# Optimization experiments

Hardware: AMD Instinct MI355X
Metric: run time of the kernel (lower is better)

Reference implementation:

```python
import jax, jax.numpy as jnp
import numpy as np

S_REF = 2        # number of reference images
C = 1024         # DINOv3 ViT-L channel dim
H = W = 64       # 1024 / patch16 feature resolution
SVD = 500        # positional subspace rank


def _l2norm(x, axis):
    return x / jnp.clip(jnp.linalg.norm(x, axis=axis, keepdims=True), 1e-12)


def setup_inputs() -> dict:
    key = jax.random.key(0)
    k1, k2, k3 = jax.random.split(key, 3)
    fmaps = jax.random.normal(k1, (1, S_REF + 1, C, H, W), jnp.float32)
    ref_masks = jax.random.randint(k2, (S_REF, H, W), 0, 2) > 0  # bool masks at feature res
    basis_raw = jax.random.normal(k3, (C, SVD), jnp.float32)
    basis, _ = jnp.linalg.qr(basis_raw)  # orthonormal positional basis, as SVD U would be
    return {"fmaps": fmaps, "ref_masks": ref_masks, "basis": basis}


def reference(fmaps, ref_masks, basis):
    S = ref_masks.shape[0]
    B, T, Cc, h, w = fmaps.shape

    # F.normalize(fmaps, p=2, dim=2)
    fn = _l2norm(fmaps, 2)
    feat_tgt = fn[0, S]  # (C,h,w) raw-normalized target feats

    # _debias_features: project onto orthogonal complement of positional subspace.
    # (I - U U^T) X computed as X - U (U^T X) to avoid a CxC matrix.
    X = fn.reshape(B * T, Cc, h * w)
    coef = jnp.einsum('ck,bcn->bkn', basis, X)          # (BT, SVD, hw)
    Xd = X - jnp.einsum('ck,bkn->bcn', basis, coef)     # (BT, C, hw)
    fd = _l2norm(Xd.reshape(B, T, Cc, h, w), 2)
    feat_refs_deb = fd[0, :S]   # (S,C,h,w)
    feat_tgt_deb = fd[0, S]     # (C,h,w)

    # Masked feature pooling -> per-reference prototype, then averaged + renormalized
    maskf = ref_masks.astype(fn.dtype)                                  # (S,h,w)
    counts = jnp.clip(maskf.sum(axis=(1, 2)), 1.0)                      # guard empty mask
    protos = jnp.einsum('schw,shw->sc', feat_refs_deb, maskf) / counts[:, None]
    ref_prototype = _l2norm(protos.mean(axis=0), 0)                     # (C,)

    # Dense ref->target cosine-similarity maps: einsum 'bchw,bcxy->bhwxy'
    sim = jnp.einsum('schw,cxy->shwxy', feat_refs_deb, feat_tgt_deb)    # (S,h,w,h,w)

    # Forward matching: target-vs-prototype similarity
    sim_fwd = jnp.einsum('cxy,c->xy', feat_tgt_deb, ref_prototype)      # (h,w)

    # Backward matching votes: for each target patch, argmax over ref patches,
    # vote if the best ref patch lies inside the reference mask.
    sim_t2r = sim.transpose(0, 3, 4, 1, 2).reshape(S, h * w, h * w)     # (S, tgt, ref)
    best_idx = jnp.argmax(sim_t2r, axis=2)                              # (S, hw)
    mask_flat = ref_masks.reshape(S, h * w)
    votes = jnp.take_along_axis(mask_flat, best_idx, axis=1).astype(jnp.int32)
    votes = votes.sum(axis=0).reshape(h, w)                             # (h,w) int32

    return sim, sim_fwd, votes
```

## Files before the change

### kernel.cpp

```cpp
#include <hip/hip_runtime.h>
#include <hip/hip_bf16.h>
#include <cfloat>

#define CH   1024
#define HW   4096
#define NSVD 500
#define TFR  3
#define SREF 2

typedef __attribute__((ext_vector_type(4))) float f32x4;
typedef __attribute__((ext_vector_type(4))) unsigned int u32x4;
typedef __attribute__((ext_vector_type(8))) short short8;


__device__ inline unsigned bfr(float x) {
  unsigned u = __float_as_uint(x);
  return (u + 0x7fffu + ((u >> 16) & 1u)) >> 16;
}
__device__ inline float lores(float x, unsigned h) {
  return x - __uint_as_float(h << 16);
}
__device__ inline float vlo(unsigned ph, unsigned pl) {
  return __uint_as_float(ph << 16) + __uint_as_float(pl << 16);
}
__device__ inline float vhi(unsigned ph, unsigned pl) {
  return __uint_as_float(ph & 0xFFFF0000u) + __uint_as_float(pl & 0xFFFF0000u);
}

__global__ __launch_bounds__(256) void normpack_k(const float* __restrict__ src,
                                                  unsigned* __restrict__ Gh,
                                                  unsigned* __restrict__ Gl,
                                                  int fbase) {
  int t = blockIdx.x >> 6;
  int n0 = (blockIdx.x & 63) * 64;
  int tid = threadIdx.x, nl = tid & 63, r = tid >> 6;
  const float* base = src + (size_t)t * CH * HW + n0 + nl;
  float s = 0.f;
  for (int c = r; c < CH; c += 4) {
    float v = base[(size_t)c * HW];
    s += v * v;
  }
  __shared__ float red[256];
  __shared__ float inv[64];
  red[tid] = s;
  __syncthreads();
  if (r == 0)
    inv[nl] = 1.0f / fmaxf(sqrtf(red[nl] + red[nl + 64] + red[nl + 128] + red[nl + 192]), 1e-12f);
  __syncthreads();

  int cg = (tid & 15) * 4;
  int n4 = n0 + cg;
  float4 w4;
  w4.x = inv[cg]; w4.y = inv[cg + 1]; w4.z = inv[cg + 2]; w4.w = inv[cg + 3];
  int gt = fbase + t;
  for (int kg = tid >> 4; kg < 128; kg += 16) {
    const float* s0 = src + ((size_t)t * CH + kg * 8) * HW + n4;
    unsigned oh[4][4], ol[4][4];
#pragma unroll
    for (int j = 0; j < 4; j++) {
      float4 va = *reinterpret_cast<const float4*>(s0 + (size_t)(2 * j) * HW);
      float4 vb = *reinterpret_cast<const float4*>(s0 + (size_t)(2 * j + 1) * HW);
      float a[4] = {va.x * w4.x, va.y * w4.y, va.z * w4.z, va.w * w4.w};
      float b[4] = {vb.x * w4.x, vb.y * w4.y, vb.z * w4.z, vb.w * w4.w};
#pragma unroll
      for (int cc = 0; cc < 4; cc++) {
        unsigned ha = bfr(a[cc]), hb = bfr(b[cc]);
        oh[cc][j] = ha | (hb << 16);
        ol[cc][j] = bfr(lores(a[cc], ha)) | (bfr(lores(b[cc], hb)) << 16);
      }
    }
    size_t vib = (((size_t)gt * 16 + (n4 >> 8)) * 128 + kg) * 256 + (n4 & 255);
#pragma unroll
    for (int cc = 0; cc < 4; cc++) {
      *reinterpret_cast<u32x4*>(Gh + (vib + cc) * 4) = *reinterpret_cast<u32x4*>(oh[cc]);
      *reinterpret_cast<u32x4*>(Gl + (vib + cc) * 4) = *reinterpret_cast<u32x4*>(ol[cc]);
    }
  }
}

__global__ __launch_bounds__(256) void scale_pack_k(const float* __restrict__ src,
                                                    const float* __restrict__ inv,
                                                    unsigned* __restrict__ Gh,
                                                    unsigned* __restrict__ Gl) {
  int gid = blockIdx.x * 256 + threadIdx.x;
  int kg = gid >> 12;
  int n = gid & 4095;
  const float* s0 = src + (size_t)(kg * 8) * HW + n;
  float w = inv[n];
  unsigned oh[4], ol[4];
#pragma unroll
  for (int j = 0; j < 4; j++) {
    float a = s0[(size_t)(2 * j) * HW] * w;
    float b = s0[(size_t)(2 * j + 1) * HW] * w;
    unsigned ha = bfr(a), hb = bfr(b);
    oh[j] = ha | (hb << 16);
    ol[j] = bfr(lores(a, ha)) | (bfr(lores(b, hb)) << 16);
  }
  size_t vi = (((size_t)(n >> 8)) * 128 + kg) * 256 + (n & 255);
  *reinterpret_cast<u32x4*>(Gh + vi * 4) = *reinterpret_cast<u32x4*>(oh);
  *reinterpret_cast<u32x4*>(Gl + vi * 4) = *reinterpret_cast<u32x4*>(ol);
}

__global__ __launch_bounds__(256) void bt_k(const float* __restrict__ bas,
                                            float* __restrict__ bt) {
  int c0 = blockIdx.x * 64;
  __shared__ float tile[64][129];
  int tid = threadIdx.x;
  for (int kc = 0; kc < 512; kc += 128) {
    for (int cr = tid >> 7; cr < 64; cr += 2) {
      int k = kc + (tid & 127);
      tile[cr][tid & 127] = (k < NSVD) ? bas[(size_t)(c0 + cr) * NSVD + k] : 0.f;
    }
    __syncthreads();
    for (int kr = tid >> 6; kr < 128; kr += 4)
      bt[(size_t)(kc + kr) * 1024 + c0 + (tid & 63)] = tile[tid & 63][kr];
    __syncthreads();
  }
}

__global__ __launch_bounds__(256) void proj_pack_k(const float* __restrict__ bt,
                                                   unsigned* __restrict__ Ah,
                                                   unsigned* __restrict__ Al) {
  int m0 = blockIdx.x * 64, n0 = blockIdx.y * 64;
  int tid = threadIdx.x;
  int tx = tid & 15, ty = tid >> 4;
  int lm = tid & 63, lk = tid >> 6;
  __shared__ float As[16][64];
  __shared__ float Bs[16][64];
  float acc[4][4] = {};
  for (int k0 = 0; k0 < 512; k0 += 16) {
#pragma unroll
    for (int i = 0; i < 4; i++) {
      int k = k0 + lk * 4 + i;
      As[lk * 4 + i][lm] = bt[(size_t)k * 1024 + m0 + lm];
      Bs[lk * 4 + i][lm] = bt[(size_t)k * 1024 + n0 + lm];
    }
    __syncthreads();
#pragma unroll
    for (int kk = 0; kk < 16; kk++) {
      float a[4], b[4];
#pragma unroll
      for (int i = 0; i < 4; i++) a[i] = As[kk][ty * 4 + i];
#pragma unroll
      for (int j = 0; j < 4; j++) b[j] = Bs[kk][tx * 4 + j];
#pragma unroll
      for (int i = 0; i < 4; i++)
#pragma unroll
        for (int j = 0; j < 4; j++) acc[i][j] += a[i] * b[j];
    }
    __syncthreads();
  }
#pragma unroll
  for (int jp = 0; jp < 2; jp++) {
    int r = n0 / 2 + tx * 2 + jp;
#pragma unroll
    for (int i = 0; i < 4; i++) {
      int c = m0 + ty * 4 + i;
      float va = ((c == 2 * r) ? 1.0f : 0.0f) - acc[i][2 * jp];
      float vb = ((c == 2 * r + 1) ? 1.0f : 0.0f) - acc[i][2 * jp + 1];
      unsigned ha = bfr(va), hb = bfr(vb);
      size_t vi = ((size_t)((c >> 8) * 128 + (r >> 2)) * 256 + (c & 255)) * 4 + (r & 3);
      Ah[vi] = ha | (hb << 16);
      Al[vi] = bfr(lores(va, ha)) | (bfr(lores(vb, hb)) << 16);
    }
  }
}

__global__ __launch_bounds__(256) void pack_basis_k(const float* __restrict__ bas,
                                                    unsigned* __restrict__ Ah,
                                                    unsigned* __restrict__ Al) {
  int r = blockIdx.x;
  for (int m = threadIdx.x; m < 512; m += 256) {
    float b0 = (m < NSVD) ? bas[(size_t)(2 * r) * NSVD + m] : 0.f;
    float b1 = (m < NSVD) ? bas[(size_t)(2 * r + 1) * NSVD + m] : 0.f;
    unsigned h0 = bfr(b0), h1 = bfr(b1);
    int c = 1024 + m;
    size_t vi = ((size_t)((c >> 8) * 128 + (r >> 2)) * 256 + (c & 255)) * 4 + (r & 3);
    Ah[vi] = h0 | (h1 << 16);
    Al[vi] = bfr(lores(b0, h0)) | (bfr(lores(b1, h1)) << 16);
  }
}

__global__ __launch_bounds__(256) void inv2_k(const float* __restrict__ pbuf,
                                              float* __restrict__ invc) {
  int i = blockIdx.x * 256 + threadIdx.x;
  int s = i >> 12, n = i & 4095;
  float s2 = 0.f;
  if (s < 2) {
#pragma unroll
    for (int j = 0; j < 4; j++) s2 += pbuf[(size_t)(s * 8 + j) * HW + n];
    s2 = sqrtf(fmaxf(1.0f - s2, 0.0f));
  } else {
#pragma unroll
    for (int j = 16; j < 24; j++) s2 += pbuf[(size_t)j * HW + n];
    s2 = sqrtf(s2);
  }
  invc[i] = 1.0f / fmaxf(s2, 1e-12f);
}

__global__ __launch_bounds__(256) void proto_k(const unsigned* __restrict__ Gh,
                                               const unsigned* __restrict__ Gl,
                                               const int* __restrict__ mask,
                                               const float* __restrict__ invc,
                                               float* __restrict__ protos,
                                               float* __restrict__ counts) {
  int s = blockIdx.x >> 7, kg = blockIdx.x & 127;
  int tid = threadIdx.x;
  const u32x4* Hv = (const u32x4*)Gh + (size_t)s * 524288;
  const u32x4* Lv = (const u32x4*)Gl + (size_t)s * 524288;
  float a[8] = {};
  int cnt = 0;
  for (int n = tid; n < HW; n += 256) {
    if (mask[s * HW + n]) {
      cnt++;
      float w = invc[s * HW + n];
      size_t vi = ((size_t)(n >> 8) * 128 + kg) * 256 + (n & 255);
      u32x4 h = Hv[vi], l = Lv[vi];
#pragma unroll
      for (int j = 0; j < 4; j++) {
        a[2 * j] += vlo(h[j], l[j]) * w;
        a[2 * j + 1] += vhi(h[j], l[j]) * w;
      }
    }
  }
  __shared__ float red[256];
  for (int e = 0; e < 8; e++) {
    red[tid] = a[e];
    __syncthreads();
    for (int o = 128; o > 0; o >>= 1) {
      if (tid < o) red[tid] += red[tid + o];
      __syncthreads();
    }
    if (tid == 0) protos[s * CH + kg * 8 + e] = red[0];
    __syncthreads();
  }
  if (kg == 0) {
    red[tid] = (float)cnt;
    __syncthreads();
    for (int o = 128; o > 0; o >>= 1) {
      if (tid < o) red[tid] += red[tid + o];
      __syncthreads();
    }
    if (tid == 0) counts[s] = fmaxf(red[0], 1.0f);
  }
}

__global__ __launch_bounds__(256) void protomv_k(const unsigned* __restrict__ Ah,
                                                 const unsigned* __restrict__ Al,
                                                 const float* __restrict__ protos,
                                                 float* __restrict__ part) {
  int s = blockIdx.x >> 2;
  int c = (blockIdx.x & 3) * 256 + threadIdx.x;
  int kc = blockIdx.y;
  __shared__ float w[128];
  if (threadIdx.x < 128) w[threadIdx.x] = protos[s * CH + kc * 128 + threadIdx.x];
  __syncthreads();
  float acc = 0.f;
  for (int rl = 0; rl < 64; rl++) {
    int r = kc * 64 + rl;
    size_t vi = ((size_t)((c >> 8) * 128 + (r >> 2)) * 256 + (c & 255)) * 4 + (r & 3);
    unsigned h = Ah[vi], l = Al[vi];
    acc += vlo(h, l) * w[2 * rl] + vhi(h, l) * w[2 * rl + 1];
  }
  part[kc * 2048 + s * CH + c] = acc;
}

__global__ __launch_bounds__(256) void protonorm_k(const float* __restrict__ part,
                                                   const float* __restrict__ counts,
                                                   float* __restrict__ proto) {
  int tid = threadIdx.x;
  __shared__ float sm[CH];
  __shared__ float red[256];
  float c0 = counts[0], c1 = counts[1];
  float ss = 0.f;
  for (int c = tid; c < CH; c += 256) {
    float p0 = 0.f, p1 = 0.f;
#pragma unroll
    for (int kc = 0; kc < 8; kc++) {
      p0 += part[kc * 2048 + c];
      p1 += part[kc * 2048 + CH + c];
    }
    float m = 0.5f * (p0 / c0 + p1 / c1);
    sm[c] = m;
    ss += m * m;
  }
  red[tid] = ss;
  __syncthreads();
  for (int o = 128; o > 0; o >>= 1) {
    if (tid < o) red[tid] += red[tid + o];
    __syncthreads();
  }
  __syncthreads();
  float inv = 1.0f / fmaxf(sqrtf(red[0]), 1e-12f);
  for (int c = tid; c < CH; c += 256) proto[c] = sm[c] * inv;
}

__global__ __launch_bounds__(256) void simfwd_k(const unsigned* __restrict__ Gh,
                                                const unsigned* __restrict__ Gl,
                                                const float* __restrict__ proto,
                                                float* __restrict__ sfpart) {
  int q = blockIdx.y;
  __shared__ float p[256];
  __shared__ float red[256];
  int tid = threadIdx.x;
  p[tid] = proto[q * 256 + tid];
  __syncthreads();
  int nl = tid & 63, sub = tid >> 6;
  int n = blockIdx.x * 64 + nl;
  const u32x4* Hv = (const u32x4*)Gh + (size_t)2 * 524288;
  const u32x4* Lv = (const u32x4*)Gl + (size_t)2 * 524288;
  float acc = 0.f;
  for (int kg = q * 32 + sub * 8; kg < q * 32 + sub * 8 + 8; kg++) {
    size_t vi = ((size_t)(n >> 8) * 128 + kg) * 256 + (n & 255);
    u32x4 h = Hv[vi], l = Lv[vi];
    int pb = (kg - q * 32) * 8;
#pragma unroll
    for (int j = 0; j < 4; j++)
      acc += vlo(h[j], l[j]) * p[pb + 2 * j] + vhi(h[j], l[j]) * p[pb + 2 * j + 1];
  }
  red[tid] = acc;
  __syncthreads();
  if (sub == 0)
    sfpart[(size_t)q * HW + n] = red[nl] + red[nl + 64] + red[nl + 128] + red[nl + 192];
}

#define G3_NT 32

__global__ __launch_bounds__(512, 2) void gemm3r_k(
    const unsigned* __restrict__ Ach, const unsigned* __restrict__ Acl,
    const unsigned* __restrict__ fh, const unsigned* __restrict__ fl,
    float* __restrict__ Xd, float* __restrict__ pbuf) {
  int orig = blockIdx.x;
  int lin = (orig & 7) * 32 + (orig >> 3);
  int z, bx, by;
  if (lin < 128) { z = lin >> 6; bx = (lin >> 4) & 3; by = lin & 15; }
  else { int l2 = lin - 128; z = 2; bx = l2 >> 4; by = l2 & 15; }
  bool isXd = (z == 2);
  int acol0 = isXd ? bx * 128 : 1024 + bx * 128;
  int acb = acol0 >> 8, aco = acol0 & 255;

  const unsigned* Agh = Ach + (size_t)acb * 131072;
  const unsigned* Agl = Acl + (size_t)acb * 131072;
  const unsigned* Bgh = fh + (size_t)z * 2097152 + (size_t)by * 131072;
  const unsigned* Bgl = fl + (size_t)z * 2097152 + (size_t)by * 131072;

  int tid = threadIdx.x, ln = tid & 63, wv = tid >> 6;
  int wr = wv >> 2, wc = wv & 3;
  int fcol = ln & 15, l16 = ln >> 4;
  int aoff = l16 * 1024 + (aco + wr * 64 + fcol) * 4;
  int boff = l16 * 1024 + (wc * 64 + fcol) * 4;

  f32x4 acc[4][4] = {};
  u32x4 ahr[4], alr[4], bhr[4], blr[4];

#define MFMA16R(A, B)                                                         \
  _Pragma("unroll")                                                           \
  for (int mf = 0; mf < 4; mf++)                                              \
    _Pragma("unroll")                                                         \
    for (int nf = 0; nf < 4; nf++)                                            \
      acc[mf][nf] = __builtin_amdgcn_mfma_f32_16x16x32_bf16(                  \
          __builtin_bit_cast(short8, A[mf]), __builtin_bit_cast(short8, B[nf]), \
          acc[mf][nf], 0, 0, 0);

#pragma unroll
  for (int mf = 0; mf < 4; mf++)
    ahr[mf] = *reinterpret_cast<const u32x4*>(Agh + aoff + mf * 64);
#pragma unroll
  for (int nf = 0; nf < 4; nf++)
    blr[nf] = *reinterpret_cast<const u32x4*>(Bgl + boff + nf * 64);
#pragma unroll
  for (int nf = 0; nf < 4; nf++)
    bhr[nf] = *reinterpret_cast<const u32x4*>(Bgh + boff + nf * 64);
#pragma unroll
  for (int mf = 0; mf < 4; mf++)
    alr[mf] = *reinterpret_cast<const u32x4*>(Agl + aoff + mf * 64);

  for (int t = 0; t < G3_NT; ++t) {
    int nxt = (t + 1) * 4096;

    __builtin_amdgcn_s_setprio(1);
    MFMA16R(ahr, bhr)
    __builtin_amdgcn_s_setprio(0);
    __builtin_amdgcn_sched_barrier(0);

    __builtin_amdgcn_s_setprio(1);
    MFMA16R(ahr, blr)
    __builtin_amdgcn_s_setprio(0);
    __builtin_amdgcn_sched_barrier(0);
    if (t + 1 < G3_NT) {
#pragma unroll
      for (int mf = 0; mf < 4; mf++)
        ahr[mf] = *reinterpret_cast<const u32x4*>(Agh + nxt + aoff + mf * 64);
#pragma unroll
      for (int nf = 0; nf < 4; nf++)
        blr[nf] = *reinterpret_cast<const u32x4*>(Bgl + nxt + boff + nf * 64);
    }
    __builtin_amdgcn_sched_barrier(0);

    __builtin_amdgcn_s_setprio(1);
    MFMA16R(alr, bhr)
    __builtin_amdgcn_s_setprio(0);
    __builtin_amdgcn_sched_barrier(0);
    if (t + 1 < G3_NT) {
#pragma unroll
      for (int nf = 0; nf < 4; nf++)
        bhr[nf] = *reinterpret_cast<const u32x4*>(Bgh + nxt + boff + nf * 64);
#pragma unroll
      for (int mf = 0; mf < 4; mf++)
        alr[mf] = *reinterpret_cast<const u32x4*>(Agl + nxt + aoff + mf * 64);
    }
    __builtin_amdgcn_sched_barrier(0);
  }
#undef MFMA16R

  int n0 = by * 256;
  float s2p[4] = {0.f, 0.f, 0.f, 0.f};
#pragma unroll
  for (int mf = 0; mf < 4; mf++) {
    int mg = bx * 128 + wr * 64 + mf * 16 + l16 * 4;
#pragma unroll
    for (int r = 0; r < 4; r++) {
#pragma unroll
      for (int nf = 0; nf < 4; nf++) {
        float v = acc[mf][nf][r];
        s2p[nf] += v * v;
        if (isXd) {
          int n = n0 + wc * 64 + nf * 16 + fcol;
          Xd[(size_t)(mg + r) * HW + n] = v;
        }
      }
    }
  }
#pragma unroll
  for (int nf = 0; nf < 4; nf++) {
    s2p[nf] += __shfl_xor(s2p[nf], 16, 64);
    s2p[nf] += __shfl_xor(s2p[nf], 32, 64);
  }
  __shared__ float sred[256];
  if (wr == 0 && l16 == 0) {
#pragma unroll
    for (int nf = 0; nf < 4; nf++) sred[wc * 64 + nf * 16 + fcol] = s2p[nf];
  }
  __syncthreads();
  if (wr == 1 && l16 == 0) {
    int slot = isXd ? 16 + bx : z * 8 + bx;
    float* dst = pbuf + (size_t)slot * HW + n0;
#pragma unroll
    for (int nf = 0; nf < 4; nf++) {
      int col = wc * 64 + nf * 16 + fcol;
      dst[col] = sred[col] + s2p[nf];
    }
  }
}

#define SIMG_NT 32

__global__ __launch_bounds__(512, 2) void simg_k(
    const unsigned* __restrict__ Gh, const unsigned* __restrict__ Gl,
    const float* __restrict__ invc, float* __restrict__ simout,
    unsigned long long* __restrict__ amg) {
  int orig = (blockIdx.z * 16 + blockIdx.y) * 16 + blockIdx.x;
  int lin = (orig & 7) * 64 + (orig >> 3);
  int z = lin >> 8, bx = (lin >> 4) & 15, by = lin & 15;

  const unsigned* Agh = Gh + (size_t)z * 2097152 + (size_t)bx * 131072;
  const unsigned* Agl = Gl + (size_t)z * 2097152 + (size_t)bx * 131072;
  const unsigned* Bgh = Gh + (size_t)2 * 2097152 + (size_t)by * 131072;
  const unsigned* Bgl = Gl + (size_t)2 * 2097152 + (size_t)by * 131072;

  int tid = threadIdx.x, ln = tid & 63, wv = tid >> 6;
  int wr = wv >> 2, wc = wv & 3;
  int fcol = ln & 15, l16 = ln >> 4;
  int aoff = l16 * 1024 + (wr * 128 + fcol) * 4;
  int boff = l16 * 1024 + (wc * 64 + fcol) * 4;

  f32x4 acc[8][4] = {};
  u32x4 ahr[8], alr[8], bhr[4], blr[4];

#define MFMA32(A, B)                                                          \
  _Pragma("unroll")                                                           \
  for (int mf = 0; mf < 8; mf++)                                              \
    _Pragma("unroll")                                                         \
    for (int nf = 0; nf < 4; nf++)                                            \
      acc[mf][nf] = __builtin_amdgcn_mfma_f32_16x16x32_bf16(                  \
          __builtin_bit_cast(short8, A[mf]), __builtin_bit_cast(short8, B[nf]), \
          acc[mf][nf], 0, 0, 0);

#pragma unroll
  for (int mf = 0; mf < 8; mf++)
    ahr[mf] = *reinterpret_cast<const u32x4*>(Agh + aoff + mf * 64);
#pragma unroll
  for (int nf = 0; nf < 4; nf++)
    blr[nf] = *reinterpret_cast<const u32x4*>(Bgl + boff + nf * 64);
#pragma unroll
  for (int nf = 0; nf < 4; nf++)
    bhr[nf] = *reinterpret_cast<const u32x4*>(Bgh + boff + nf * 64);
#pragma unroll
  for (int mf = 0; mf < 8; mf++)
    alr[mf] = *reinterpret_cast<const u32x4*>(Agl + aoff + mf * 64);

  for (int t = 0; t < SIMG_NT; ++t) {
    int nxt = (t + 1) * 4096;

    __builtin_amdgcn_s_setprio(1);
    MFMA32(ahr, bhr)
    __builtin_amdgcn_s_setprio(0);
    __builtin_amdgcn_sched_barrier(0);

    __builtin_amdgcn_s_setprio(1);
    MFMA32(ahr, blr)
    __builtin_amdgcn_s_setprio(0);
    __builtin_amdgcn_sched_barrier(0);
    if (t + 1 < SIMG_NT) {
#pragma unroll
      for (int mf = 0; mf < 8; mf++)
        ahr[mf] = *reinterpret_cast<const u32x4*>(Agh + nxt + aoff + mf * 64);
#pragma unroll
      for (int nf = 0; nf < 4; nf++)
        blr[nf] = *reinterpret_cast<const u32x4*>(Bgl + nxt + boff + nf * 64);
    }
    __builtin_amdgcn_sched_barrier(0);

    __builtin_amdgcn_s_setprio(1);
    MFMA32(alr, bhr)
    __builtin_amdgcn_s_setprio(0);
    __builtin_amdgcn_sched_barrier(0);
    if (t + 1 < SIMG_NT) {
#pragma unroll
      for (int nf = 0; nf < 4; nf++)
        bhr[nf] = *reinterpret_cast<const u32x4*>(Bgh + nxt + boff + nf * 64);
#pragma unroll
      for (int mf = 0; mf < 8; mf++)
        alr[mf] = *reinterpret_cast<const u32x4*>(Agl + nxt + aoff + mf * 64);
    }
    __builtin_amdgcn_sched_barrier(0);
  }
#undef MFMA32

  const float* rs = invc + (size_t)z * HW;
  float* C = simout + (size_t)z * HW * HW;
  unsigned long long* am = amg + (size_t)z * HW;
  int m0 = bx * 256, n0 = by * 256;
  int ncol[4];
#pragma unroll
  for (int nf = 0; nf < 4; nf++) ncol[nf] = n0 + wc * 64 + nf * 16 + fcol;
  float bv[4] = {-FLT_MAX, -FLT_MAX, -FLT_MAX, -FLT_MAX};
  int bi[4] = {0, 0, 0, 0};
#pragma unroll
  for (int mf = 0; mf < 8; mf++) {
    int mg = m0 + wr * 128 + mf * 16 + l16 * 4;
#pragma unroll
    for (int r = 0; r < 4; r++) {
      float sc = rs[mg + r];
#pragma unroll
      for (int nf = 0; nf < 4; nf++) {
        float val = acc[mf][nf][r] * sc;
        C[(size_t)(mg + r) * HW + ncol[nf]] = val;
        if (val > bv[nf]) { bv[nf] = val; bi[nf] = mg + r; }
      }
    }
  }
#pragma unroll
  for (int nf = 0; nf < 4; nf++) {
#pragma unroll
    for (int st = 16; st <= 32; st <<= 1) {
      float ov = __shfl_xor(bv[nf], st, 64);
      int oi = __shfl_xor(bi[nf], st, 64);
      if (ov > bv[nf] || (ov == bv[nf] && oi < bi[nf])) { bv[nf] = ov; bi[nf] = oi; }
    }
  }
  if (ln < 16) {
#pragma unroll
    for (int nf = 0; nf < 4; nf++) {
      unsigned b = __float_as_uint(bv[nf]);
      unsigned key = (b & 0x80000000u) ? ~b : (b | 0x80000000u);
      unsigned long long packed =
          ((unsigned long long)key << 32) | (unsigned)(~bi[nf]);
      atomicMax(am + ncol[nf], packed);
    }
  }
}

__global__ __launch_bounds__(256) void votes_k(const unsigned long long* __restrict__ am,
                                               const int* __restrict__ mask,
                                               const float* __restrict__ sfpart,
                                               float* __restrict__ simfwd,
                                               float* __restrict__ out) {
  int xy = blockIdx.x * 256 + threadIdx.x;
  simfwd[xy] = ((sfpart[xy] + sfpart[HW + xy]) + sfpart[2 * HW + xy]) + sfpart[3 * HW + xy];
  int vote = 0;
  for (int s = 0; s < SREF; s++) {
    unsigned long long p = am[(size_t)s * HW + xy];
    int bi = (int)(~(unsigned)p);
    vote += (mask[s * HW + bi] != 0);
  }
  out[xy] = (float)vote;
}

extern "C" void kernel_launch(void* const* d_in, const int* in_sizes, int n_in,
                              void* d_out, int out_size, void* d_ws, size_t ws_size,
                              hipStream_t stream) {
  const float* fmaps = (const float*)d_in[0];
  const int* mask = (const int*)d_in[1];
  const float* basis = (const float*)d_in[2];
  float* out = (float*)d_out;
  float* ws = (float*)d_ws;

  unsigned* fh = (unsigned*)ws;
  unsigned* fl = (unsigned*)(ws + 6291456);
  float* invc = ws + 12595200;
  float* protos = ws + 12607552;
  float* proto = ws + 12611648;
  unsigned long long* am = (unsigned long long*)(ws + 12612672);
  float* part = ws + 12629056;
  float* counts = ws + 12645440;
  float* sfpart = ws + 12645504;

  float* sim = out;
  float* simfwd = out + 33554432;
  float* votes = out + 33558528;
  unsigned* Ach = (unsigned*)out;
  unsigned* Acl = (unsigned*)(out + 786432);
  float* bt = out + 1572864;
  float* Xd = out + 5767168;
  float* pbuf = out + 9961472;

  hipMemsetAsync(am, 0, (size_t)SREF * HW * sizeof(unsigned long long), stream);

  normpack_k<<<dim3(TFR * 64), 256, 0, stream>>>(fmaps, fh, fl, 0);

  bt_k<<<dim3(16), 256, 0, stream>>>(basis, bt);
  proj_pack_k<<<dim3(16, 16), 256, 0, stream>>>(bt, Ach, Acl);
  pack_basis_k<<<dim3(512), 256, 0, stream>>>(basis, Ach, Acl);

  gemm3r_k<<<dim3(256), 512, 0, stream>>>(Ach, Acl, fh, fl, Xd, pbuf);
  inv2_k<<<dim3(48), 256, 0, stream>>>(pbuf, invc);

  scale_pack_k<<<dim3(2048), 256, 0, stream>>>(Xd, invc + 2 * HW,
                                               fh + (size_t)2 * 2097152,
                                               fl + (size_t)2 * 2097152);

  proto_k<<<256, 256, 0, stream>>>(fh, fl, mask, invc, protos, counts);
  protomv_k<<<dim3(8, 8), 256, 0, stream>>>(Ach, Acl, protos, part);
  protonorm_k<<<1, 256, 0, stream>>>(part, counts, proto);

  simfwd_k<<<dim3(64, 4), 256, 0, stream>>>(fh, fl, proto, sfpart);

  simg_k<<<dim3(16, 16, 2), 512, 0, stream>>>(fh, fl, invc, sim, am);

  votes_k<<<16, 256, 0, stream>>>(am, mask, sfpart, simfwd, votes);
}
```

Before: 408.5 us.

## Fuse target debias output packing into GEMM epilogue and defer column normalization

The projection GEMM epilogue now writes the debiased target features directly as packed bf16 hi/lo split instead of storing fp32 Xd, which removes the separate scale_pack kernel and the fp32 round trip through memory. The target's inverse-norm scaling is moved out of the packed data and applied later as a per-column factor in the similarity epilogue and the forward-match output. The target is normalized into a separate buffer so the GEMM can overwrite its own slot. The risk is a small numerical change, because the unnormalized values are split into bf16 pairs before scaling, and the direct writes from the MFMA fragment layout may be less coalesced.

```diff
diff --git a/kernel.cpp b/kernel.cpp
--- a/kernel.cpp
+++ b/kernel.cpp
@@ -9,6 +9,7 @@
 #define SREF 2
 
 typedef __attribute__((ext_vector_type(4))) float f32x4;
+typedef __attribute__((ext_vector_type(2))) unsigned int u32x2;
 typedef __attribute__((ext_vector_type(4))) unsigned int u32x4;
 typedef __attribute__((ext_vector_type(8))) short short8;
 
@@ -76,29 +77,6 @@
       *reinterpret_cast<u32x4*>(Gl + (vib + cc) * 4) = *reinterpret_cast<u32x4*>(ol[cc]);
     }
   }
-}
-
-__global__ __launch_bounds__(256) void scale_pack_k(const float* __restrict__ src,
-                                                    const float* __restrict__ inv,
-                                                    unsigned* __restrict__ Gh,
-                                                    unsigned* __restrict__ Gl) {
-  int gid = blockIdx.x * 256 + threadIdx.x;
-  int kg = gid >> 12;
-  int n = gid & 4095;
-  const float* s0 = src + (size_t)(kg * 8) * HW + n;
-  float w = inv[n];
-  unsigned oh[4], ol[4];
-#pragma unroll
-  for (int j = 0; j < 4; j++) {
-    float a = s0[(size_t)(2 * j) * HW] * w;
-    float b = s0[(size_t)(2 * j + 1) * HW] * w;
-    unsigned ha = bfr(a), hb = bfr(b);
-    oh[j] = ha | (hb << 16);
-    ol[j] = bfr(lores(a, ha)) | (bfr(lores(b, hb)) << 16);
-  }
-  size_t vi = (((size_t)(n >> 8)) * 128 + kg) * 256 + (n & 255);
-  *reinterpret_cast<u32x4*>(Gh + vi * 4) = *reinterpret_cast<u32x4*>(oh);
-  *reinterpret_cast<u32x4*>(Gl + vi * 4) = *reinterpret_cast<u32x4*>(ol);
 }
 
 __global__ __launch_bounds__(256) void bt_k(const float* __restrict__ bas,
@@ -328,8 +306,9 @@
 
 __global__ __launch_bounds__(512, 2) void gemm3r_k(
     const unsigned* __restrict__ Ach, const unsigned* __restrict__ Acl,
-    const unsigned* __restrict__ fh, const unsigned* __restrict__ fl,
-    float* __restrict__ Xd, float* __restrict__ pbuf) {
+    unsigned* __restrict__ fh, unsigned* __restrict__ fl,
+    const unsigned* __restrict__ TgtH, const unsigned* __restrict__ TgtL,
+    float* __restrict__ pbuf) {
   int orig = blockIdx.x;
   int lin = (orig & 7) * 32 + (orig >> 3);
   int z, bx, by;
@@ -341,8 +320,10 @@
 
   const unsigned* Agh = Ach + (size_t)acb * 131072;
   const unsigned* Agl = Acl + (size_t)acb * 131072;
-  const unsigned* Bgh = fh + (size_t)z * 2097152 + (size_t)by * 131072;
-  const unsigned* Bgl = fl + (size_t)z * 2097152 + (size_t)by * 131072;
+  const unsigned* Bgh = isXd ? TgtH + (size_t)by * 131072
+                             : fh + (size_t)z * 2097152 + (size_t)by * 131072;
+  const unsigned* Bgl = isXd ? TgtL + (size_t)by * 131072
+                             : fl + (size_t)z * 2097152 + (size_t)by * 131072;
 
   int tid = threadIdx.x, ln = tid & 63, wv = tid >> 6;
   int wr = wv >> 2, wc = wv & 3;
@@ -414,20 +395,26 @@
 #undef MFMA16R
 
   int n0 = by * 256;
+  unsigned* Gh2 = fh + (size_t)2 * 2097152;
+  unsigned* Gl2 = fl + (size_t)2 * 2097152;
   float s2p[4] = {0.f, 0.f, 0.f, 0.f};
 #pragma unroll
   for (int mf = 0; mf < 4; mf++) {
-    int mg = bx * 128 + wr * 64 + mf * 16 + l16 * 4;
-#pragma unroll
-    for (int r = 0; r < 4; r++) {
-#pragma unroll
-      for (int nf = 0; nf < 4; nf++) {
-        float v = acc[mf][nf][r];
-        s2p[nf] += v * v;
-        if (isXd) {
-          int n = n0 + wc * 64 + nf * 16 + fcol;
-          Xd[(size_t)(mg + r) * HW + n] = v;
-        }
+    int kpb = bx * 64 + wr * 32 + mf * 8 + l16 * 2;
+#pragma unroll
+    for (int nf = 0; nf < 4; nf++) {
+      float v0 = acc[mf][nf][0], v1 = acc[mf][nf][1];
+      float v2 = acc[mf][nf][2], v3 = acc[mf][nf][3];
+      s2p[nf] += v0 * v0 + v1 * v1 + v2 * v2 + v3 * v3;
+      if (isXd) {
+        int n = n0 + wc * 64 + nf * 16 + fcol;
+        unsigned h0 = bfr(v0), h1 = bfr(v1), h2 = bfr(v2), h3 = bfr(v3);
+        u32x2 oh = {h0 | (h1 << 16), h2 | (h3 << 16)};
+        u32x2 ol = {bfr(lores(v0, h0)) | (bfr(lores(v1, h1)) << 16),
+                    bfr(lores(v2, h2)) | (bfr(lores(v3, h3)) << 16)};
+        size_t vi = ((size_t)((n >> 8) * 128 + (kpb >> 2)) * 256 + (n & 255)) * 4 + (kpb & 3);
+        *reinterpret_cast<u32x2*>(Gh2 + vi) = oh;
+        *reinterpret_cast<u32x2*>(Gl2 + vi) = ol;
       }
     }
   }
@@ -538,12 +525,17 @@
 #undef MFMA32
 
   const float* rs = invc + (size_t)z * HW;
+  const float* cs = invc + (size_t)2 * HW;
   float* C = simout + (size_t)z * HW * HW;
   unsigned long long* am = amg + (size_t)z * HW;
   int m0 = bx * 256, n0 = by * 256;
   int ncol[4];
-#pragma unroll
-  for (int nf = 0; nf < 4; nf++) ncol[nf] = n0 + wc * 64 + nf * 16 + fcol;
+  float csv[4];
+#pragma unroll
+  for (int nf = 0; nf < 4; nf++) {
+    ncol[nf] = n0 + wc * 64 + nf * 16 + fcol;
+    csv[nf] = cs[ncol[nf]];
+  }
   float bv[4] = {-FLT_MAX, -FLT_MAX, -FLT_MAX, -FLT_MAX};
   int bi[4] = {0, 0, 0, 0};
 #pragma unroll
@@ -554,7 +546,7 @@
       float sc = rs[mg + r];
 #pragma unroll
       for (int nf = 0; nf < 4; nf++) {
-        float val = acc[mf][nf][r] * sc;
+        float val = acc[mf][nf][r] * sc * csv[nf];
         C[(size_t)(mg + r) * HW + ncol[nf]] = val;
         if (val > bv[nf]) { bv[nf] = val; bi[nf] = mg + r; }
       }
@@ -584,10 +576,12 @@
 __global__ __launch_bounds__(256) void votes_k(const unsigned long long* __restrict__ am,
                                                const int* __restrict__ mask,
                                                const float* __restrict__ sfpart,
+                                               const float* __restrict__ invc,
                                                float* __restrict__ simfwd,
                                                float* __restrict__ out) {
   int xy = blockIdx.x * 256 + threadIdx.x;
-  simfwd[xy] = ((sfpart[xy] + sfpart[HW + xy]) + sfpart[2 * HW + xy]) + sfpart[3 * HW + xy];
+  float sf = ((sfpart[xy] + sfpart[HW + xy]) + sfpart[2 * HW + xy]) + sfpart[3 * HW + xy];
+  simfwd[xy] = sf * invc[2 * HW + xy];
   int vote = 0;
   for (int s = 0; s < SREF; s++) {
     unsigned long long p = am[(size_t)s * HW + xy];
@@ -622,23 +616,21 @@
   unsigned* Ach = (unsigned*)out;
   unsigned* Acl = (unsigned*)(out + 786432);
   float* bt = out + 1572864;
-  float* Xd = out + 5767168;
+  unsigned* TgtH = (unsigned*)(out + 5767168);
+  unsigned* TgtL = (unsigned*)(out + 7864320);
   float* pbuf = out + 9961472;
 
   hipMemsetAsync(am, 0, (size_t)SREF * HW * sizeof(unsigned long long), stream);
 
-  normpack_k<<<dim3(TFR * 64), 256, 0, stream>>>(fmaps, fh, fl, 0);
+  normpack_k<<<dim3(SREF * 64), 256, 0, stream>>>(fmaps, fh, fl, 0);
+  normpack_k<<<dim3(64), 256, 0, stream>>>(fmaps + (size_t)2 * CH * HW, TgtH, TgtL, 0);
 
   bt_k<<<dim3(16), 256, 0, stream>>>(basis, bt);
   proj_pack_k<<<dim3(16, 16), 256, 0, stream>>>(bt, Ach, Acl);
   pack_basis_k<<<dim3(512), 256, 0, stream>>>(basis, Ach, Acl);
 
-  gemm3r_k<<<dim3(256), 512, 0, stream>>>(Ach, Acl, fh, fl, Xd, pbuf);
+  gemm3r_k<<<dim3(256), 512, 0, stream>>>(Ach, Acl, fh, fl, TgtH, TgtL, pbuf);
   inv2_k<<<dim3(48), 256, 0, stream>>>(pbuf, invc);
-
-  scale_pack_k<<<dim3(2048), 256, 0, stream>>>(Xd, invc + 2 * HW,
-                                               fh + (size_t)2 * 2097152,
-                                               fl + (size_t)2 * 2097152);
 
   proto_k<<<256, 256, 0, stream>>>(fh, fl, mask, invc, protos, counts);
   protomv_k<<<dim3(8, 8), 256, 0, stream>>>(Ach, Acl, protos, part);
@@ -648,5 +640,5 @@
 
   simg_k<<<dim3(16, 16, 2), 512, 0, stream>>>(fh, fl, invc, sim, am);
 
-  votes_k<<<16, 256, 0, stream>>>(am, mask, sfpart, simfwd, votes);
-}
+  votes_k<<<16, 256, 0, stream>>>(am, mask, sfpart, invc, simfwd, votes);
+}
```

After: 478.7 us. 1.17x slower.
